# Performance work log

Hardware: AMD Instinct MI355X
Metric: run time of the kernel (lower is better)

## Reference

```python
import jax, jax.numpy as jnp
import numpy as np

B, N, DIM, H, R = 8, 4096, 256, 8, 32


def setup_inputs() -> dict:
    key = jax.random.key(0)
    k0, k1, k2, k3 = jax.random.split(key, 4)
    x = jax.random.normal(k0, (B, N, DIM), jnp.float32)
    # Dense qkv: in=dim, out=dim*2*num_heads
    qkv_w = jax.random.normal(k1, (DIM, 2 * H * DIM), jnp.float32) * 0.02
    qkv_b = jnp.zeros((2 * H * DIM,), jnp.float32)
    # learned low-rank 'lunchbox' projection (GlorotUniform-ish scale)
    lunchbox = jax.random.normal(k2, (DIM, R), jnp.float32) * (1.0 / np.sqrt(DIM))
    # Dense proj: in=num_heads*dim, out=dim
    proj_w = jax.random.normal(k3, (H * DIM, DIM), jnp.float32) * 0.02
    proj_b = jnp.zeros((DIM,), jnp.float32)
    return dict(x=x, qkv_w=qkv_w, qkv_b=qkv_b, lunchbox=lunchbox,
                proj_w=proj_w, proj_b=proj_b)


def reference(x, qkv_w, qkv_b, lunchbox, proj_w, proj_b):
    Bsz, Nseq, C = x.shape
    D, Rr = lunchbox.shape            # (dim, lunchbox_dim)
    Hh = qkv_w.shape[1] // (2 * D)    # num_heads
    scale = max(D, Rr) ** -0.5

    h = x @ qkv_w + qkv_b                                   # (B, N, 2*H*D)
    h = jnp.transpose(h, (0, 2, 1)).reshape(Bsz, 2, Hh, D, Nseq)
    q, v = h[:, 0], h[:, 1]                                 # (B, H, D, N)

    # einsum('bikj,kr->birk'): reduce over sequence j, keep dim k elementwise
    attn = jnp.einsum('bhdn,dr->bhrd', q, lunchbox) * scale  # (B, H, R, D)
    # NOTE: original TF code calls tf.nn.softmax(attn, -1) but DISCARDS the
    # result (unassigned) -- faithfully reproduced as a no-op here.

    # einsum('birk,bikn->bink'): reduce over lunchbox rank r
    res = jnp.einsum('bhrd,bhdn->bhnd', attn, v)             # (B, H, N, D)

    # raw reshape (NOT a transpose), exactly as in the TF source
    out = res.reshape(Bsz, Nseq, Hh * D) @ proj_w + proj_b   # (B, N, dim)
    return out
```

## Files before the change

### kernel.cpp

```cpp
#include <hip/hip_runtime.h>
#include <stdint.h>

typedef unsigned short u16;
typedef unsigned int u32;
typedef __attribute__((ext_vector_type(8))) short short8;
typedef __attribute__((ext_vector_type(4))) float f32x4;

#define B_    8
#define N_    4096
#define DIM_  256
#define HD_   2048
#define NQKV_ 4096

__device__ __forceinline__ float bf2f(u16 u) {
  union { u32 u; float f; } v; v.u = ((u32)u) << 16; return v.f;
}
__device__ __forceinline__ u16 f2bf(float f) {
  union { float f; u32 u; } v; v.f = f;
  u32 r = v.u + 0x7fffu + ((v.u >> 16) & 1u);
  return (u16)(r >> 16);
}
__device__ __forceinline__ float ldin(const void* p, size_t i, int isbf) {
  return isbf ? bf2f(((const u16*)p)[i]) : ((const float*)p)[i];
}
__device__ __forceinline__ void load16_to_lds(const u16* gsrc, u16* ldst) {
  auto gp = (const __attribute__((address_space(1))) void*)(uintptr_t)gsrc;
  auto lp = (__attribute__((address_space(3))) void*)(uintptr_t)ldst;
  __builtin_amdgcn_global_load_lds(gp, lp, 16, 0, 0);
}
__device__ __forceinline__ int probe_isbf(const void* x) {
  u32 w = ((const u32*)x)[threadIdx.x & 63];
  int e = (int)((w >> 7) & 0xff);
  unsigned long long m = __ballot(e >= 118 && e <= 130);
  return __popcll(m) >= 32;
}

__global__ void cvtprep_kernel(const void* __restrict__ x, const void* __restrict__ qkv_w,
                               const void* __restrict__ proj_w, const void* __restrict__ qkv_b,
                               const void* __restrict__ proj_b, const void* __restrict__ lunchbox,
                               u16* __restrict__ xb, float* __restrict__ part,
                               u16* __restrict__ wv, u16* __restrict__ pt,
                               float* __restrict__ Psum, float* __restrict__ qb,
                               float* __restrict__ pbv, float* __restrict__ Lsum) {
  int isbf = probe_isbf(x);
  int bid = blockIdx.x, t = threadIdx.x;
  __shared__ float sm[8][256];
  __shared__ float tile[32][33];
  if (bid < 1024) {
    int b = bid >> 7, ch = bid & 127;
    int c8 = (t & 31) * 8, rg = t >> 5;
    float s[8] = {0.f, 0.f, 0.f, 0.f, 0.f, 0.f, 0.f, 0.f};
#pragma unroll
    for (int i = 0; i < 4; ++i) {
      int row = rg * 4 + i;
      size_t off = ((size_t)b * N_ + (size_t)ch * 32 + row) * DIM_ + c8;
      if (isbf) {
        short8 v = *(const short8*)((const u16*)x + off);
        *(short8*)(xb + off) = v;
#pragma unroll
        for (int j = 0; j < 8; ++j) s[j] += bf2f((u16)v[j]);
      } else {
        f32x4 a = *(const f32x4*)((const float*)x + off);
        f32x4 bb = *(const f32x4*)((const float*)x + off + 4);
        short8 o;
        o[0] = (short)f2bf(a[0]); o[1] = (short)f2bf(a[1]);
        o[2] = (short)f2bf(a[2]); o[3] = (short)f2bf(a[3]);
        o[4] = (short)f2bf(bb[0]); o[5] = (short)f2bf(bb[1]);
        o[6] = (short)f2bf(bb[2]); o[7] = (short)f2bf(bb[3]);
        *(short8*)(xb + off) = o;
        s[0] += a[0]; s[1] += a[1]; s[2] += a[2]; s[3] += a[3];
        s[4] += bb[0]; s[5] += bb[1]; s[6] += bb[2]; s[7] += bb[3];
      }
    }
#pragma unroll
    for (int j = 0; j < 8; ++j) sm[rg][c8 + j] = s[j];
    __syncthreads();
    float tot = 0.f;
#pragma unroll
    for (int r = 0; r < 8; ++r) tot += sm[r][t];
    part[(b * 128 + ch) * DIM_ + t] = tot;
  } else if (bid < 1280) {
    size_t i = ((size_t)(bid - 1024) * 256 + t) * 8;
    int k = (int)(i >> 11), e = (int)(i & 2047);
    size_t src = (size_t)k * NQKV_ + HD_ + e;
    short8 o;
#pragma unroll
    for (int j = 0; j < 8; ++j) o[j] = (short)f2bf(ldin(qkv_w, src + j, isbf));
    *(short8*)&wv[i] = o;
  } else if (bid < 1792) {
    int bid2 = bid - 1280;
    int c0 = (bid2 & 7) * 32, e0 = (bid2 >> 3) * 32;
    int tx = t & 31, ty = t >> 5;
    for (int i = ty; i < 32; i += 8)
      tile[i][tx] = ldin(proj_w, (size_t)(e0 + i) * 256 + c0 + tx, isbf);
    __syncthreads();
    for (int i = ty; i < 32; i += 8)
      pt[(size_t)(c0 + i) * HD_ + e0 + tx] = f2bf(tile[tx][i]);
  } else if (bid < 2048) {
    int d = bid - 1792;
    float s = 0.f;
    for (int jj = 0; jj < 8; ++jj) s += ldin(proj_w, (size_t)(jj * 256 + d) * 256 + t, isbf);
    Psum[d * 256 + t] = s;
  } else if (bid < 2064) {
    int i = (bid - 2048) * 256 + t;
    qb[i] = ldin(qkv_b, i, isbf);
  } else if (bid == 2064) {
    pbv[t] = ldin(proj_b, t, isbf);
  } else {
    float s = 0.f;
    for (int r = 0; r < 32; ++r) s += ldin(lunchbox, (size_t)t * 32 + r, isbf);
    Lsum[t] = s;
  }
}

__global__ void gpart_kernel(const void* __restrict__ xraw, const void* __restrict__ qkv_w,
                             const float* __restrict__ part, float* __restrict__ gpart) {
  int isbf = probe_isbf(xraw);
  int bid = blockIdx.x, t = threadIdx.x;
  int kc = bid & 3, hc = (bid >> 2) & 7, b = bid >> 5;
  __shared__ float red[4][64];
  __shared__ float xs[64];
  {
    int col = t & 63, q = t >> 6;
    float s = 0.f;
    for (int i = 0; i < 32; ++i)
      s += part[(b * 128 + q * 32 + i) * 256 + kc * 64 + col];
    red[q][col] = s;
  }
  __syncthreads();
  if (t < 64) xs[t] = red[0][t] + red[1][t] + red[2][t] + red[3][t];
  __syncthreads();
  int hd = hc * 256 + t;
  float s = 0.f;
#pragma unroll 8
  for (int i = 0; i < 64; ++i)
    s += xs[i] * ldin(qkv_w, (size_t)(kc * 64 + i) * NQKV_ + hd, isbf);
  gpart[kc * 16384 + b * HD_ + hd] = s;
}

__global__ void gfin_kernel(const float* __restrict__ gpart, const float* __restrict__ qb,
                            const float* __restrict__ Lsum, const float* __restrict__ Psum,
                            float* __restrict__ g, float* __restrict__ rcpart) {
  int bid = blockIdx.x, t = threadIdx.x;
  int ds = bid & 3, bh = bid >> 2;
  int b = bh >> 3, h = bh & 7;
  __shared__ float us[64];
  if (t < 64) {
    int d = ds * 64 + t, hd = h * 256 + d;
    float sum = gpart[b * HD_ + hd] + gpart[16384 + b * HD_ + hd] +
                gpart[32768 + b * HD_ + hd] + gpart[49152 + b * HD_ + hd];
    float gg = 0.0625f * (sum + 4096.0f * qb[hd]) * Lsum[d];
    g[b * HD_ + hd] = gg;
    us[t] = gg * qb[HD_ + hd];
  }
  __syncthreads();
  float r = 0.f;
#pragma unroll 8
  for (int i = 0; i < 64; ++i)
    r += us[i] * Psum[(ds * 64 + i) * 256 + t];
  rcpart[ds * 16384 + bh * 256 + t] = r;
}

__global__ void wgscale_kernel(const u16* __restrict__ wv, const float* __restrict__ g,
                               u16* __restrict__ wg) {
  int b = blockIdx.x >> 8;
  size_t i = ((size_t)(blockIdx.x & 255) * 256 + threadIdx.x) * 8;
  int e = (int)(i & 2047);
  short8 w8 = *(const short8*)&wv[i];
  f32x4 g0 = *(const f32x4*)&g[b * HD_ + e];
  f32x4 g1 = *(const f32x4*)&g[b * HD_ + e + 4];
  short8 o;
  o[0] = (short)f2bf(bf2f((u16)w8[0]) * g0[0]);
  o[1] = (short)f2bf(bf2f((u16)w8[1]) * g0[1]);
  o[2] = (short)f2bf(bf2f((u16)w8[2]) * g0[2]);
  o[3] = (short)f2bf(bf2f((u16)w8[3]) * g0[3]);
  o[4] = (short)f2bf(bf2f((u16)w8[4]) * g1[0]);
  o[5] = (short)f2bf(bf2f((u16)w8[5]) * g1[1]);
  o[6] = (short)f2bf(bf2f((u16)w8[6]) * g1[2]);
  o[7] = (short)f2bf(bf2f((u16)w8[7]) * g1[3]);
  *(short8*)&wg[(size_t)b * 524288 + i] = o;
}

__global__ __launch_bounds__(512, 2) void stage1_kernel(
    const u16* __restrict__ pt, const u16* __restrict__ wg,
    u16* __restrict__ Mt, int b0, int nblk) {
  __shared__ alignas(16) char smem[65536];
  float* eps = (float*)smem;

  int bid = blockIdx.x;
  int sid = (bid & 7) * (nblk >> 3) + (bid >> 3);
  int c0i = sid & 1, k0i = (sid >> 1) & 1, jj = (sid >> 2) & 7;
  int h = (sid >> 5) & 7, bb = sid >> 8;
  int b = b0 + bb;
  int c0 = c0i * 128, k0 = k0i * 128;
  const int panel = bb * 8 + h;
  const u16* Abase = pt + (size_t)c0 * HD_ + jj * 256;
  const u16* Bbase = wg + (size_t)b * 524288 + (size_t)k0 * HD_ + h * 256;

  const int t = threadIdx.x;
  const int grp = t >> 8, tt = t & 255;
  const int lane = tt & 63, wave = tt >> 6;
  const int wr = wave >> 1, wc = wave & 1;
  char* aB0 = smem + grp * 32768;
  char* aB1 = aB0 + 16384;

  f32x4 acc[4][4] = {};

#define S1_STAGE(i_, dst_)                                                          \
  {                                                                                 \
    int dcol = ((i_) * 2 + grp) * 32;                                               \
    _Pragma("unroll") for (int it = 0; it < 2; ++it) {                              \
      int idx = it * 256 + tt, row = idx >> 2, slot = idx & 3;                      \
      int sc = dcol + ((slot ^ ((row >> 1) & 3)) * 8);                              \
      load16_to_lds(Abase + (size_t)row * HD_ + sc, (u16*)(dst_) + idx * 8);        \
      load16_to_lds(Bbase + (size_t)row * HD_ + sc,                                 \
                    (u16*)((char*)(dst_) + 8192) + idx * 8);                        \
    }                                                                               \
  }
#define S1_COMP(buf_)                                                               \
  {                                                                                 \
    const u16* lA = (const u16*)(buf_);                                             \
    const u16* lB = (const u16*)((char*)(buf_) + 8192);                             \
    short8 af[4], bfr[4];                                                           \
    _Pragma("unroll") for (int mi = 0; mi < 4; ++mi) {                              \
      int row = wr * 64 + mi * 16 + (lane & 15);                                    \
      af[mi] = *(const short8*)&lA[row * 32 + (((lane >> 4) ^ ((row >> 1) & 3)) * 8)]; \
    }                                                                               \
    _Pragma("unroll") for (int ni = 0; ni < 4; ++ni) {                              \
      int row = wc * 64 + ni * 16 + (lane & 15);                                    \
      bfr[ni] = *(const short8*)&lB[row * 32 + (((lane >> 4) ^ ((row >> 1) & 3)) * 8)]; \
    }                                                                               \
    _Pragma("unroll") for (int mi = 0; mi < 4; ++mi)                                \
      _Pragma("unroll") for (int ni = 0; ni < 4; ++ni)                              \
        acc[mi][ni] = __builtin_amdgcn_mfma_f32_16x16x32_bf16(af[mi], bfr[ni],      \
                                                              acc[mi][ni], 0, 0, 0); \
  }

  S1_STAGE(0, aB0);
  __syncthreads();
#pragma unroll 1
  for (int ii = 0; ii < 2; ++ii) {
    S1_STAGE(ii * 2 + 1, aB1);
    S1_COMP(aB0);
    __syncthreads();
    if (ii < 1) S1_STAGE(ii * 2 + 2, aB0);
    S1_COMP(aB1);
    __syncthreads();
  }

  const int rl = t >> 4, cc = (t & 15) * 8;
#pragma unroll
  for (int mi = 0; mi < 4; ++mi) {
    __syncthreads();
    if (grp == 0) {
#pragma unroll
      for (int ni = 0; ni < 4; ++ni) {
        f32x4 v = acc[mi][ni];
        int re = wr * 16 + (lane >> 4) * 4, ce = wc * 64 + ni * 16 + (lane & 15);
        eps[(re + 0) * 128 + ce] = v[0];
        eps[(re + 1) * 128 + ce] = v[1];
        eps[(re + 2) * 128 + ce] = v[2];
        eps[(re + 3) * 128 + ce] = v[3];
      }
    }
    __syncthreads();
    if (grp == 1) {
#pragma unroll
      for (int ni = 0; ni < 4; ++ni) {
        f32x4 v = acc[mi][ni];
        int re = wr * 16 + (lane >> 4) * 4, ce = wc * 64 + ni * 16 + (lane & 15);
        eps[(re + 0) * 128 + ce] += v[0];
        eps[(re + 1) * 128 + ce] += v[1];
        eps[(re + 2) * 128 + ce] += v[2];
        eps[(re + 3) * 128 + ce] += v[3];
      }
    }
    __syncthreads();
    int rowloc = (rl >> 4) * 64 + mi * 16 + (rl & 15);
    alignas(16) u16 pk[8];
#pragma unroll
    for (int j = 0; j < 8; ++j) pk[j] = f2bf(eps[rl * 128 + cc + j]);
    u16* dst = Mt + (size_t)panel * 524288 + (size_t)(c0 + rowloc) * HD_ + jj * 256 + k0 + cc;
    *(short8*)dst = *(short8*)pk;
  }
}

__global__ __launch_bounds__(512, 4) void stage2_kernel(
    const void* __restrict__ xraw, const u16* __restrict__ xb, const u16* __restrict__ Mt,
    const float* __restrict__ rcpart, const float* __restrict__ pbv,
    void* __restrict__ outv, int b0, int nblk) {
  __shared__ alignas(16) char smem[65536];
  float* eps = (float*)smem;

  int bid = blockIdx.x;
  int sid = (bid & 7) * (nblk >> 3) + (bid >> 3);
  int ct = sid & 1, rt = (sid >> 1) & 3, h = (sid >> 3) & 7, bb = sid >> 6;
  int b = b0 + bb;
  int nn0 = rt * 128, c0 = ct * 128;
  const int panel = bb * 8 + h;
  const u16* Abase = xb + (size_t)b * 1048576 + (size_t)nn0 * HD_;
  const u16* Bbase = Mt + (size_t)panel * 524288 + (size_t)c0 * HD_;

  const int t = threadIdx.x;
  const int grp = t >> 8, tt = t & 255;
  const int lane = tt & 63, wave = tt >> 6;
  const int wr = wave >> 1, wc = wave & 1;
  char* aB0 = smem + grp * 32768;
  char* aB1 = aB0 + 16384;

  f32x4 acc[4][4] = {};

#define S2_STAGE(i_, dst_)                                                          \
  {                                                                                 \
    int kcol = ((i_) * 2 + grp) * 32;                                               \
    _Pragma("unroll") for (int it = 0; it < 2; ++it) {                              \
      int idx = it * 256 + tt, row = idx >> 2, slot = idx & 3;                      \
      int sc = kcol + ((slot ^ ((row >> 1) & 3)) * 8);                              \
      load16_to_lds(Abase + (size_t)row * HD_ + sc, (u16*)(dst_) + idx * 8);        \
      load16_to_lds(Bbase + (size_t)row * HD_ + sc,                                 \
                    (u16*)((char*)(dst_) + 8192) + idx * 8);                        \
    }                                                                               \
  }
#define S2_COMP(buf_)                                                               \
  {                                                                                 \
    const u16* lA = (const u16*)(buf_);                                             \
    const u16* lB = (const u16*)((char*)(buf_) + 8192);                             \
    short8 af[4], bfr[4];                                                           \
    _Pragma("unroll") for (int mi = 0; mi < 4; ++mi) {                              \
      int row = wr * 64 + mi * 16 + (lane & 15);                                    \
      af[mi] = *(const short8*)&lA[row * 32 + (((lane >> 4) ^ ((row >> 1) & 3)) * 8)]; \
    }                                                                               \
    _Pragma("unroll") for (int ni = 0; ni < 4; ++ni) {                              \
      int row = wc * 64 + ni * 16 + (lane & 15);                                    \
      bfr[ni] = *(const short8*)&lB[row * 32 + (((lane >> 4) ^ ((row >> 1) & 3)) * 8)]; \
    }                                                                               \
    _Pragma("unroll") for (int mi = 0; mi < 4; ++mi)                                \
      _Pragma("unroll") for (int ni = 0; ni < 4; ++ni)                              \
        acc[mi][ni] = __builtin_amdgcn_mfma_f32_16x16x32_bf16(af[mi], bfr[ni],      \
                                                              acc[mi][ni], 0, 0, 0); \
  }

  S2_STAGE(0, aB0);
  __syncthreads();
#pragma unroll 1
  for (int ii = 0; ii < 16; ++ii) {
    S2_STAGE(ii * 2 + 1, aB1);
    S2_COMP(aB0);
    __syncthreads();
    if (ii < 15) S2_STAGE(ii * 2 + 2, aB0);
    S2_COMP(aB1);
    __syncthreads();
  }

  int isbf = probe_isbf(xraw);
  const int rl = t >> 4, cc = (t & 15) * 8;
  float rc[8];
  {
    const float* rp = rcpart + (size_t)(b * 8 + h) * 256 + c0 + cc;
    const float* pb = pbv + c0 + cc;
#pragma unroll
    for (int j = 0; j < 8; ++j)
      rc[j] = rp[j] + rp[16384 + j] + rp[32768 + j] + rp[49152 + j] + pb[j];
  }
#pragma unroll
  for (int mi = 0; mi < 4; ++mi) {
    __syncthreads();
    if (grp == 0) {
#pragma unroll
      for (int ni = 0; ni < 4; ++ni) {
        f32x4 v = acc[mi][ni];
        int re = wr * 16 + (lane >> 4) * 4, ce = wc * 64 + ni * 16 + (lane & 15);
        eps[(re + 0) * 128 + ce] = v[0];
        eps[(re + 1) * 128 + ce] = v[1];
        eps[(re + 2) * 128 + ce] = v[2];
        eps[(re + 3) * 128 + ce] = v[3];
      }
    }
    __syncthreads();
    if (grp == 1) {
#pragma unroll
      for (int ni = 0; ni < 4; ++ni) {
        f32x4 v = acc[mi][ni];
        int re = wr * 16 + (lane >> 4) * 4, ce = wc * 64 + ni * 16 + (lane & 15);
        eps[(re + 0) * 128 + ce] += v[0];
        eps[(re + 1) * 128 + ce] += v[1];
        eps[(re + 2) * 128 + ce] += v[2];
        eps[(re + 3) * 128 + ce] += v[3];
      }
    }
    __syncthreads();
    int grow = b * N_ + h * 512 + nn0 + (rl >> 4) * 64 + mi * 16 + (rl & 15);
    if (isbf) {
      alignas(16) u16 pk[8];
#pragma unroll
      for (int j = 0; j < 8; ++j) pk[j] = f2bf(eps[rl * 128 + cc + j] + rc[j]);
      *(short8*)((u16*)outv + (size_t)grow * 256 + c0 + cc) = *(short8*)pk;
    } else {
      float* op = (float*)outv + (size_t)grow * 256 + c0 + cc;
      f32x4 o0, o1;
      o0[0] = eps[rl * 128 + cc + 0] + rc[0];
      o0[1] = eps[rl * 128 + cc + 1] + rc[1];
      o0[2] = eps[rl * 128 + cc + 2] + rc[2];
      o0[3] = eps[rl * 128 + cc + 3] + rc[3];
      o1[0] = eps[rl * 128 + cc + 4] + rc[4];
      o1[1] = eps[rl * 128 + cc + 5] + rc[5];
      o1[2] = eps[rl * 128 + cc + 6] + rc[6];
      o1[3] = eps[rl * 128 + cc + 7] + rc[7];
      ((f32x4*)op)[0] = o0;
      ((f32x4*)op)[1] = o1;
    }
  }
}

extern "C" void kernel_launch(void* const* d_in, const int* in_sizes, int n_in,
                              void* d_out, int out_size, void* d_ws, size_t ws_size,
                              hipStream_t stream) {
  const void* x        = d_in[0];
  const void* qkv_w    = d_in[1];
  const void* qkv_b    = d_in[2];
  const void* lunchbox = d_in[3];
  const void* proj_w   = d_in[4];
  const void* proj_b   = d_in[5];
  char* ws = (char*)d_ws;

  u16*   xbuf   = (u16*)(ws + 0);
  u16*   wv     = (u16*)(ws + 16777216);
  u16*   pt     = (u16*)(ws + 17825792);
  float* part   = (float*)(ws + 18874368);
  float* g      = (float*)(ws + 19922944);
  float* gpart  = (float*)(ws + 19988480);
  float* rcpart = (float*)(ws + 20250624);
  float* Psum   = (float*)(ws + 20512768);
  float* qb     = (float*)(ws + 20774912);
  float* pbv    = (float*)(ws + 20791296);
  float* Lsum   = (float*)(ws + 20792320);
  u16*   wg     = (u16*)(ws + 20971520);
  u16*   Mt     = (u16*)(ws + 29360128);

  cvtprep_kernel<<<2066, 256, 0, stream>>>(x, qkv_w, proj_w, qkv_b, proj_b, lunchbox,
                                           xbuf, part, wv, pt, Psum, qb, pbv, Lsum);
  gpart_kernel<<<256, 256, 0, stream>>>(x, qkv_w, part, gpart);
  gfin_kernel<<<256, 256, 0, stream>>>(gpart, qb, Lsum, Psum, g, rcpart);
  wgscale_kernel<<<2048, 256, 0, stream>>>(wv, g, wg);

  size_t mt_off = 29360128;
  int gb = 8;
  while (gb > 1 && mt_off + (size_t)gb * 8388608 > ws_size) gb >>= 1;
  for (int b0 = 0; b0 < 8; b0 += gb) {
    stage1_kernel<<<gb * 256, 512, 0, stream>>>(pt, wg, Mt, b0, gb * 256);
    stage2_kernel<<<gb * 64, 512, 0, stream>>>(x, xbuf, Mt, rcpart, pbv, d_out, b0, gb * 64);
  }
}
```

Baseline: 105.1 us.

## Replace split-K two-group GEMM with single-group four-buffer async pipeline

Both GEMM stages drop the two 256-thread groups that each handled half of K and were then reduced through LDS. Each block now uses 256 threads running the full K loop over a 4-slot LDS ring, with loads issued two tiles ahead and explicit vmcnt waits plus a single barrier per tile. The epilogue no longer needs the cross-group add pass, and each thread writes 16 outputs instead of 8. The intent is to overlap global loads with MFMA work and remove the split-K reduction and extra barriers. In exchange each block has half as many waves, which lowers the parallelism available to hide latency.

New measurement: 109.7 us. 1.04x slower.

```diff
diff --git a/kernel.cpp b/kernel.cpp
--- a/kernel.cpp
+++ b/kernel.cpp
@@ -181,43 +181,18 @@
   *(short8*)&wg[(size_t)b * 524288 + i] = o;
 }
 
-__global__ __launch_bounds__(512, 2) void stage1_kernel(
-    const u16* __restrict__ pt, const u16* __restrict__ wg,
-    u16* __restrict__ Mt, int b0, int nblk) {
-  __shared__ alignas(16) char smem[65536];
-  float* eps = (float*)smem;
-
-  int bid = blockIdx.x;
-  int sid = (bid & 7) * (nblk >> 3) + (bid >> 3);
-  int c0i = sid & 1, k0i = (sid >> 1) & 1, jj = (sid >> 2) & 7;
-  int h = (sid >> 5) & 7, bb = sid >> 8;
-  int b = b0 + bb;
-  int c0 = c0i * 128, k0 = k0i * 128;
-  const int panel = bb * 8 + h;
-  const u16* Abase = pt + (size_t)c0 * HD_ + jj * 256;
-  const u16* Bbase = wg + (size_t)b * 524288 + (size_t)k0 * HD_ + h * 256;
-
-  const int t = threadIdx.x;
-  const int grp = t >> 8, tt = t & 255;
-  const int lane = tt & 63, wave = tt >> 6;
-  const int wr = wave >> 1, wc = wave & 1;
-  char* aB0 = smem + grp * 32768;
-  char* aB1 = aB0 + 16384;
-
-  f32x4 acc[4][4] = {};
-
-#define S1_STAGE(i_, dst_)                                                          \
+#define PIPE_STAGE(Abase_, Bbase_, kt_, dst_)                                       \
   {                                                                                 \
-    int dcol = ((i_) * 2 + grp) * 32;                                               \
+    int kcol = (kt_) * 32;                                                          \
     _Pragma("unroll") for (int it = 0; it < 2; ++it) {                              \
-      int idx = it * 256 + tt, row = idx >> 2, slot = idx & 3;                      \
-      int sc = dcol + ((slot ^ ((row >> 1) & 3)) * 8);                              \
-      load16_to_lds(Abase + (size_t)row * HD_ + sc, (u16*)(dst_) + idx * 8);        \
-      load16_to_lds(Bbase + (size_t)row * HD_ + sc,                                 \
+      int idx = it * 256 + t, row = idx >> 2, slot = idx & 3;                       \
+      int sc = kcol + ((slot ^ ((row >> 1) & 3)) * 8);                              \
+      load16_to_lds((Abase_) + (size_t)row * HD_ + sc, (u16*)(dst_) + idx * 8);     \
+      load16_to_lds((Bbase_) + (size_t)row * HD_ + sc,                              \
                     (u16*)((char*)(dst_) + 8192) + idx * 8);                        \
     }                                                                               \
   }
-#define S1_COMP(buf_)                                                               \
+#define PIPE_COMP(buf_)                                                             \
   {                                                                                 \
     const u16* lA = (const u16*)(buf_);                                             \
     const u16* lB = (const u16*)((char*)(buf_) + 8192);                             \
@@ -235,57 +210,74 @@
         acc[mi][ni] = __builtin_amdgcn_mfma_f32_16x16x32_bf16(af[mi], bfr[ni],      \
                                                               acc[mi][ni], 0, 0, 0); \
   }
-
-  S1_STAGE(0, aB0);
-  __syncthreads();
+#define PIPE_ITER(Abase_, Bbase_, kt_, nb_, KI_)                                    \
+  {                                                                                 \
+    if ((kt_) < (KI_)-2) PIPE_STAGE(Abase_, Bbase_, (kt_) + 2, smem + (nb_) * 16384); \
+    if ((kt_) < (KI_)-2)       { asm volatile("s_waitcnt vmcnt(8)" ::: "memory"); } \
+    else if ((kt_) == (KI_)-2) { asm volatile("s_waitcnt vmcnt(4)" ::: "memory"); } \
+    else                       { asm volatile("s_waitcnt vmcnt(0)" ::: "memory"); } \
+    __builtin_amdgcn_s_barrier();                                                   \
+    __builtin_amdgcn_sched_barrier(0);                                              \
+    PIPE_COMP(smem + ((kt_) & 3) * 16384);                                          \
+  }
+
+__global__ __launch_bounds__(256, 2) void stage1_kernel(
+    const u16* __restrict__ pt, const u16* __restrict__ wg,
+    u16* __restrict__ Mt, int b0, int nblk) {
+  __shared__ alignas(16) char smem[65536];
+  float* eps = (float*)smem;
+
+  int bid = blockIdx.x;
+  int sid = (bid & 7) * (nblk >> 3) + (bid >> 3);
+  int cq = sid & 1, kq = (sid >> 1) & 1, jj = (sid >> 2) & 7;
+  int h = (sid >> 5) & 7, bb = sid >> 8;
+  int b = b0 + bb;
+  int c0 = cq * 128, k0 = kq * 128;
+  const int panel = bb * 8 + h;
+  const u16* Abase = pt + (size_t)c0 * HD_ + jj * 256;
+  const u16* Bbase = wg + (size_t)b * 524288 + (size_t)k0 * HD_ + h * 256;
+
+  const int t = threadIdx.x, lane = t & 63, wave = t >> 6;
+  const int wr = wave >> 1, wc = wave & 1;
+
+  f32x4 acc[4][4] = {};
+
+  PIPE_STAGE(Abase, Bbase, 0, smem);
+  PIPE_STAGE(Abase, Bbase, 1, smem + 16384);
 #pragma unroll 1
-  for (int ii = 0; ii < 2; ++ii) {
-    S1_STAGE(ii * 2 + 1, aB1);
-    S1_COMP(aB0);
-    __syncthreads();
-    if (ii < 1) S1_STAGE(ii * 2 + 2, aB0);
-    S1_COMP(aB1);
-    __syncthreads();
-  }
-
-  const int rl = t >> 4, cc = (t & 15) * 8;
+  for (int u = 0; u < 2; ++u) {
+    int k4 = u * 4;
+    PIPE_ITER(Abase, Bbase, k4 + 0, 2, 8);
+    PIPE_ITER(Abase, Bbase, k4 + 1, 3, 8);
+    PIPE_ITER(Abase, Bbase, k4 + 2, 0, 8);
+    PIPE_ITER(Abase, Bbase, k4 + 3, 1, 8);
+  }
+
+  const int rl = t >> 3, cc = (t & 7) * 16;
 #pragma unroll
   for (int mi = 0; mi < 4; ++mi) {
     __syncthreads();
-    if (grp == 0) {
-#pragma unroll
-      for (int ni = 0; ni < 4; ++ni) {
-        f32x4 v = acc[mi][ni];
-        int re = wr * 16 + (lane >> 4) * 4, ce = wc * 64 + ni * 16 + (lane & 15);
-        eps[(re + 0) * 128 + ce] = v[0];
-        eps[(re + 1) * 128 + ce] = v[1];
-        eps[(re + 2) * 128 + ce] = v[2];
-        eps[(re + 3) * 128 + ce] = v[3];
-      }
+#pragma unroll
+    for (int ni = 0; ni < 4; ++ni) {
+      f32x4 v = acc[mi][ni];
+      int re = wr * 16 + (lane >> 4) * 4, ce = wc * 64 + ni * 16 + (lane & 15);
+      eps[(re + 0) * 128 + ce] = v[0];
+      eps[(re + 1) * 128 + ce] = v[1];
+      eps[(re + 2) * 128 + ce] = v[2];
+      eps[(re + 3) * 128 + ce] = v[3];
     }
     __syncthreads();
-    if (grp == 1) {
-#pragma unroll
-      for (int ni = 0; ni < 4; ++ni) {
-        f32x4 v = acc[mi][ni];
-        int re = wr * 16 + (lane >> 4) * 4, ce = wc * 64 + ni * 16 + (lane & 15);
-        eps[(re + 0) * 128 + ce] += v[0];
-        eps[(re + 1) * 128 + ce] += v[1];
-        eps[(re + 2) * 128 + ce] += v[2];
-        eps[(re + 3) * 128 + ce] += v[3];
-      }
-    }
-    __syncthreads();
     int rowloc = (rl >> 4) * 64 + mi * 16 + (rl & 15);
-    alignas(16) u16 pk[8];
-#pragma unroll
-    for (int j = 0; j < 8; ++j) pk[j] = f2bf(eps[rl * 128 + cc + j]);
+    alignas(16) u16 pk[16];
+#pragma unroll
+    for (int j = 0; j < 16; ++j) pk[j] = f2bf(eps[rl * 128 + cc + j]);
     u16* dst = Mt + (size_t)panel * 524288 + (size_t)(c0 + rowloc) * HD_ + jj * 256 + k0 + cc;
     *(short8*)dst = *(short8*)pk;
-  }
-}
-
-__global__ __launch_bounds__(512, 4) void stage2_kernel(
+    *(short8*)(dst + 8) = *(short8*)(pk + 8);
+  }
+}
+
+__global__ __launch_bounds__(256, 2) void stage2_kernel(
     const void* __restrict__ xraw, const u16* __restrict__ xb, const u16* __restrict__ Mt,
     const float* __restrict__ rcpart, const float* __restrict__ pbv,
     void* __restrict__ outv, int b0, int nblk) {
@@ -301,113 +293,64 @@
   const u16* Abase = xb + (size_t)b * 1048576 + (size_t)nn0 * HD_;
   const u16* Bbase = Mt + (size_t)panel * 524288 + (size_t)c0 * HD_;
 
-  const int t = threadIdx.x;
-  const int grp = t >> 8, tt = t & 255;
-  const int lane = tt & 63, wave = tt >> 6;
+  const int t = threadIdx.x, lane = t & 63, wave = t >> 6;
   const int wr = wave >> 1, wc = wave & 1;
-  char* aB0 = smem + grp * 32768;
-  char* aB1 = aB0 + 16384;
 
   f32x4 acc[4][4] = {};
 
-#define S2_STAGE(i_, dst_)                                                          \
-  {                                                                                 \
-    int kcol = ((i_) * 2 + grp) * 32;                                               \
-    _Pragma("unroll") for (int it = 0; it < 2; ++it) {                              \
-      int idx = it * 256 + tt, row = idx >> 2, slot = idx & 3;                      \
-      int sc = kcol + ((slot ^ ((row >> 1) & 3)) * 8);                              \
-      load16_to_lds(Abase + (size_t)row * HD_ + sc, (u16*)(dst_) + idx * 8);        \
-      load16_to_lds(Bbase + (size_t)row * HD_ + sc,                                 \
-                    (u16*)((char*)(dst_) + 8192) + idx * 8);                        \
-    }                                                                               \
-  }
-#define S2_COMP(buf_)                                                               \
-  {                                                                                 \
-    const u16* lA = (const u16*)(buf_);                                             \
-    const u16* lB = (const u16*)((char*)(buf_) + 8192);                             \
-    short8 af[4], bfr[4];                                                           \
-    _Pragma("unroll") for (int mi = 0; mi < 4; ++mi) {                              \
-      int row = wr * 64 + mi * 16 + (lane & 15);                                    \
-      af[mi] = *(const short8*)&lA[row * 32 + (((lane >> 4) ^ ((row >> 1) & 3)) * 8)]; \
-    }                                                                               \
-    _Pragma("unroll") for (int ni = 0; ni < 4; ++ni) {                              \
-      int row = wc * 64 + ni * 16 + (lane & 15);                                    \
-      bfr[ni] = *(const short8*)&lB[row * 32 + (((lane >> 4) ^ ((row >> 1) & 3)) * 8)]; \
-    }                                                                               \
-    _Pragma("unroll") for (int mi = 0; mi < 4; ++mi)                                \
-      _Pragma("unroll") for (int ni = 0; ni < 4; ++ni)                              \
-        acc[mi][ni] = __builtin_amdgcn_mfma_f32_16x16x32_bf16(af[mi], bfr[ni],      \
-                                                              acc[mi][ni], 0, 0, 0); \
-  }
-
-  S2_STAGE(0, aB0);
-  __syncthreads();
+  PIPE_STAGE(Abase, Bbase, 0, smem);
+  PIPE_STAGE(Abase, Bbase, 1, smem + 16384);
 #pragma unroll 1
-  for (int ii = 0; ii < 16; ++ii) {
-    S2_STAGE(ii * 2 + 1, aB1);
-    S2_COMP(aB0);
-    __syncthreads();
-    if (ii < 15) S2_STAGE(ii * 2 + 2, aB0);
-    S2_COMP(aB1);
-    __syncthreads();
+  for (int u = 0; u < 16; ++u) {
+    int k4 = u * 4;
+    PIPE_ITER(Abase, Bbase, k4 + 0, 2, 64);
+    PIPE_ITER(Abase, Bbase, k4 + 1, 3, 64);
+    PIPE_ITER(Abase, Bbase, k4 + 2, 0, 64);
+    PIPE_ITER(Abase, Bbase, k4 + 3, 1, 64);
   }
 
   int isbf = probe_isbf(xraw);
-  const int rl = t >> 4, cc = (t & 15) * 8;
-  float rc[8];
+  const int rl = t >> 3, cc = (t & 7) * 16;
+  float rc[16];
   {
     const float* rp = rcpart + (size_t)(b * 8 + h) * 256 + c0 + cc;
     const float* pb = pbv + c0 + cc;
 #pragma unroll
-    for (int j = 0; j < 8; ++j)
+    for (int j = 0; j < 16; ++j)
       rc[j] = rp[j] + rp[16384 + j] + rp[32768 + j] + rp[49152 + j] + pb[j];
   }
 #pragma unroll
   for (int mi = 0; mi < 4; ++mi) {
     __syncthreads();
-    if (grp == 0) {
-#pragma unroll
-      for (int ni = 0; ni < 4; ++ni) {
-        f32x4 v = acc[mi][ni];
-        int re = wr * 16 + (lane >> 4) * 4, ce = wc * 64 + ni * 16 + (lane & 15);
-        eps[(re + 0) * 128 + ce] = v[0];
-        eps[(re + 1) * 128 + ce] = v[1];
-        eps[(re + 2) * 128 + ce] = v[2];
-        eps[(re + 3) * 128 + ce] = v[3];
-      }
-    }
-    __syncthreads();
-    if (grp == 1) {
-#pragma unroll
-      for (int ni = 0; ni < 4; ++ni) {
-        f32x4 v = acc[mi][ni];
-        int re = wr * 16 + (lane >> 4) * 4, ce = wc * 64 + ni * 16 + (lane & 15);
-        eps[(re + 0) * 128 + ce] += v[0];
-        eps[(re + 1) * 128 + ce] += v[1];
-        eps[(re + 2) * 128 + ce] += v[2];
-        eps[(re + 3) * 128 + ce] += v[3];
-      }
+#pragma unroll
+    for (int ni = 0; ni < 4; ++ni) {
+      f32x4 v = acc[mi][ni];
+      int re = wr * 16 + (lane >> 4) * 4, ce = wc * 64 + ni * 16 + (lane & 15);
+      eps[(re + 0) * 128 + ce] = v[0];
+      eps[(re + 1) * 128 + ce] = v[1];
+      eps[(re + 2) * 128 + ce] = v[2];
+      eps[(re + 3) * 128 + ce] = v[3];
     }
     __syncthreads();
     int grow = b * N_ + h * 512 + nn0 + (rl >> 4) * 64 + mi * 16 + (rl & 15);
     if (isbf) {
-      alignas(16) u16 pk[8];
-#pragma unroll
-      for (int j = 0; j < 8; ++j) pk[j] = f2bf(eps[rl * 128 + cc + j] + rc[j]);
-      *(short8*)((u16*)outv + (size_t)grow * 256 + c0 + cc) = *(short8*)pk;
+      alignas(16) u16 pk[16];
+#pragma unroll
+      for (int j = 0; j < 16; ++j) pk[j] = f2bf(eps[rl * 128 + cc + j] + rc[j]);
+      u16* op = (u16*)outv + (size_t)grow * 256 + c0 + cc;
+      *(short8*)op = *(short8*)pk;
+      *(short8*)(op + 8) = *(short8*)(pk + 8);
     } else {
       float* op = (float*)outv + (size_t)grow * 256 + c0 + cc;
-      f32x4 o0, o1;
-      o0[0] = eps[rl * 128 + cc + 0] + rc[0];
-      o0[1] = eps[rl * 128 + cc + 1] + rc[1];
-      o0[2] = eps[rl * 128 + cc + 2] + rc[2];
-      o0[3] = eps[rl * 128 + cc + 3] + rc[3];
-      o1[0] = eps[rl * 128 + cc + 4] + rc[4];
-      o1[1] = eps[rl * 128 + cc + 5] + rc[5];
-      o1[2] = eps[rl * 128 + cc + 6] + rc[6];
-      o1[3] = eps[rl * 128 + cc + 7] + rc[7];
-      ((f32x4*)op)[0] = o0;
-      ((f32x4*)op)[1] = o1;
+#pragma unroll
+      for (int chv = 0; chv < 4; ++chv) {
+        f32x4 o_;
+        o_[0] = eps[rl * 128 + cc + chv * 4 + 0] + rc[chv * 4 + 0];
+        o_[1] = eps[rl * 128 + cc + chv * 4 + 1] + rc[chv * 4 + 1];
+        o_[2] = eps[rl * 128 + cc + chv * 4 + 2] + rc[chv * 4 + 2];
+        o_[3] = eps[rl * 128 + cc + chv * 4 + 3] + rc[chv * 4 + 3];
+        ((f32x4*)op)[chv] = o_;
+      }
     }
   }
 }
@@ -447,7 +390,7 @@
   int gb = 8;
   while (gb > 1 && mt_off + (size_t)gb * 8388608 > ws_size) gb >>= 1;
   for (int b0 = 0; b0 < 8; b0 += gb) {
-    stage1_kernel<<<gb * 256, 512, 0, stream>>>(pt, wg, Mt, b0, gb * 256);
-    stage2_kernel<<<gb * 64, 512, 0, stream>>>(x, xbuf, Mt, rcpart, pbv, d_out, b0, gb * 64);
-  }
-}
+    stage1_kernel<<<gb * 256, 256, 0, stream>>>(pt, wg, Mt, b0, gb * 256);
+    stage2_kernel<<<gb * 64, 256, 0, stream>>>(x, xbuf, Mt, rcpart, pbv, d_out, b0, gb * 64);
+  }
+}
```
